# Kernel optimization log

Hardware: AMD Instinct MI355X
Metric: run time of the kernel (lower is better)

Reference implementation:

```python
import jax, jax.numpy as jnp
import numpy as np

HEAD_DIM = 64

def setup_inputs() -> dict:
    key = jax.random.key(0)
    k1, k2, k3 = jax.random.split(key, 3)
    B, L, D = 2, 2048, 1024
    x = jax.random.normal(k1, (B, L, D), dtype=jnp.float32)
    # torch nn.Linear weights are [out_features, in_features]
    w_qkv = jax.random.normal(k2, (3 * D, D), dtype=jnp.float32) * (D ** -0.5)
    w_out = jax.random.normal(k3, (D, D), dtype=jnp.float32) * (D ** -0.5)
    # causal mask: True = attend (masked_fill on logical_not)
    mask = jnp.tril(jnp.ones((L, L), dtype=bool))[None].repeat(B, axis=0)
    return {"x": x, "mask": mask, "w_qkv": w_qkv, "w_out": w_out}

def reference(x, mask, w_qkv, w_out):
    B, L, D = x.shape
    H, Hd = D // HEAD_DIM, HEAD_DIM
    scale = Hd ** -0.5
    qkv = x @ w_qkv.T                               # [B, L, 3D]
    q, k, v = jnp.split(qkv, 3, axis=-1)
    # [B, L, D] -> [B, H, L, Hd]
    def split_heads(t):
        return t.reshape(B, L, H, Hd).transpose(0, 2, 1, 3)
    q, k, v = split_heads(q), split_heads(k), split_heads(v)
    attn = jnp.einsum('bhld,bhmd->bhlm', q, k) * scale  # [B, H, L, L]
    attn = jnp.where(mask[:, None, :, :], attn, -jnp.inf)
    attn = jax.nn.softmax(attn, axis=-1)
    out = jnp.einsum('bhlm,bhmd->bhld', attn, v)        # [B, H, L, Hd]
    out = out.transpose(0, 2, 1, 3).reshape(B, L, D)
    return out @ w_out.T
```

## Files before the change

### kernel.cpp

```cpp
#include <hip/hip_runtime.h>
#include <hip/hip_bf16.h>


typedef __bf16 bf16;
typedef __bf16 bf16x8 __attribute__((ext_vector_type(8)));
typedef __bf16 bf16x4 __attribute__((ext_vector_type(4)));
typedef float  f32x4  __attribute__((ext_vector_type(4)));

#define MFMA16(a, b, c) __builtin_amdgcn_mfma_f32_16x16x32_bf16(a, b, c, 0, 0, 0)

__global__ __launch_bounds__(256) void cvt_all(
    const float* __restrict__ x, const float* __restrict__ wq,
    const float* __restrict__ wo, bf16* __restrict__ dst) {
  int i = blockIdx.x * 256 + threadIdx.x;
  const float* src;
  int off;
  if (i < 1048576) {
    src = x; off = i;
  } else if (i < 1048576 + 786432) {
    src = wq; off = i - 1048576;
  } else {
    src = wo; off = i - (1048576 + 786432);
  }
  float4 v = ((const float4*)src)[off];
  bf16x4 o;
  o[0] = (bf16)v.x; o[1] = (bf16)v.y; o[2] = (bf16)v.z; o[3] = (bf16)v.w;
  ((bf16x4*)dst)[i] = o;
}

__device__ __forceinline__ void gload_lds16(const bf16* g, bf16* l) {
  __builtin_amdgcn_global_load_lds(
      (const __attribute__((address_space(1))) void*)g,
      (__attribute__((address_space(3))) void*)l, 16, 0, 0);
}

template <int ROWS>
__device__ __forceinline__ void stage_tile(const bf16* __restrict__ src, int ld,
                                           bf16* lds, int tid) {
  const int wid = tid >> 6;
#pragma unroll
  for (int i = 0; i < ROWS / 32; ++i) {
    int c = i * 256 + tid;
    int row = c >> 3;
    int slot = (c & 7) ^ (row & 7);
    gload_lds16(src + row * ld + slot * 8, lds + i * 2048 + wid * 512);
  }
}

__device__ __forceinline__ void stage_tile512(const bf16* __restrict__ src,
                                              int ld, bf16* lds, int tid) {
  int row = tid >> 3;
  int slot = (tid & 7) ^ (row & 7);
  gload_lds16(src + row * ld + slot * 8, lds + (tid >> 6) * 512);
}

__device__ __forceinline__ bf16x8 read_swz(const bf16* lds, int row, int kbyte) {
  int byte = row * 128 + (kbyte ^ ((row & 7) << 4));
  return *(const bf16x8*)((const char*)lds + byte);
}

template <int MODE>
__global__ __launch_bounds__(256) void gemm_nt(
    const bf16* __restrict__ A, const bf16* __restrict__ Bt,
    bf16* __restrict__ C0, bf16* __restrict__ C1, bf16* __restrict__ C2,
    float* __restrict__ Cf,
    int M, int N, int K, int nbm) {
  __shared__ bf16 ldsA[128 * 64];
  __shared__ bf16 ldsB[128 * 64];
  const int tid = threadIdx.x;
  const int lane = tid & 63, wid = tid >> 6;
  const int wr = wid >> 1, wc = wid & 1;
  const int bm = blockIdx.x % nbm, bn = blockIdx.x / nbm;
  const int l15 = lane & 15, g = lane >> 4;

  f32x4 acc[4][4] = {};
  const bf16* Ab = A + (size_t)bm * 128 * K;
  const bf16* Bb = Bt + (size_t)bn * 128 * K;

  for (int k0 = 0; k0 < K; k0 += 64) {
    __syncthreads();
    stage_tile<128>(Ab + k0, K, ldsA, tid);
    stage_tile<128>(Bb + k0, K, ldsB, tid);
    __syncthreads();
#pragma unroll
    for (int kc = 0; kc < 2; ++kc) {
      bf16x8 af[4], bfr[4];
#pragma unroll
      for (int mi = 0; mi < 4; ++mi)
        af[mi] = read_swz(ldsA, wr * 64 + mi * 16 + l15, kc * 64 + g * 16);
#pragma unroll
      for (int ni = 0; ni < 4; ++ni)
        bfr[ni] = read_swz(ldsB, wc * 64 + ni * 16 + l15, kc * 64 + g * 16);
#pragma unroll
      for (int mi = 0; mi < 4; ++mi)
#pragma unroll
        for (int ni = 0; ni < 4; ++ni)
          acc[mi][ni] = MFMA16(af[mi], bfr[ni], acc[mi][ni]);
    }
  }

  const int mbase = bm * 128 + wr * 64, nbase = bn * 128 + wc * 64;
#pragma unroll
  for (int mi = 0; mi < 4; ++mi) {
#pragma unroll
    for (int ni = 0; ni < 4; ++ni) {
#pragma unroll
      for (int r = 0; r < 4; ++r) {
        int m = mbase + mi * 16 + g * 4 + r;
        int n = nbase + ni * 16 + l15;
        if (MODE == 0) {
          Cf[(size_t)m * N + n] = acc[mi][ni][r];
        } else {
          bf16 v = (bf16)acc[mi][ni][r];
          int part = n >> 10;
          int hh = (n >> 6) & 15, hd = n & 63;
          int bb = m >> 11, ll = m & 2047;
          size_t bhb = (size_t)(bb * 16 + hh);
          if (part == 2) {
            C2[(bhb * 64 + hd) * 2048 + ll] = v;
          } else {
            bf16* dst = (part == 0) ? C0 : C1;
            dst[(bhb * 2048 + ll) * 64 + hd] = v;
          }
        }
      }
    }
  }
}

__global__ __launch_bounds__(512) void attn_fwd8(
    const bf16* __restrict__ Q, const bf16* __restrict__ Kb,
    const bf16* __restrict__ Vt, bf16* __restrict__ O2) {
  __shared__ bf16 ldsK[2][64 * 64];
  __shared__ bf16 ldsVt[2][64 * 64];
  __shared__ bf16 ldsP[8 * 1024];

  const int tid = threadIdx.x, lane = tid & 63, wid = tid >> 6;
  const int l15 = lane & 15, g = lane >> 4;
  const int wsub = wid & 3;
  const int half = wid >> 2;
  const int qpair = 15 - (blockIdx.x >> 5);
  const int bh = blockIdx.x & 31;
  const int b = bh >> 4, h = bh & 15;
  const bf16* Qh  = Q  + (size_t)bh * 2048 * 64;
  const bf16* Kh  = Kb + (size_t)bh * 2048 * 64;
  const bf16* VtH = Vt + (size_t)bh * 64 * 2048;
  const int qbase = qpair * 128;
  const int qrow = qbase + half * 64 + wsub * 16 + l15;
  const int myqt = 2 * qpair + half;
  const int nt = 2 * qpair + 2;

  int off_rd[4][2];
#pragma unroll
  for (int r4 = 0; r4 < 4; ++r4)
#pragma unroll
    for (int dk = 0; dk < 2; ++dk)
      off_rd[r4][dk] = (r4 * 16 + l15) * 128 +
                       ((dk * 64 + g * 16) ^ ((l15 & 7) << 4));
  int off_pw[4];
#pragma unroll
  for (int s4 = 0; s4 < 4; ++s4)
    off_pw[s4] = l15 * 128 + ((s4 * 32 + g * 8) ^ ((l15 & 7) << 4));
  char* Pw = (char*)&ldsP[wid * 1024];

  bf16x8 qf[2];
#pragma unroll
  for (int dk = 0; dk < 2; ++dk)
    qf[dk] = *(const bf16x8*)(Qh + (size_t)qrow * 64 + dk * 32 + g * 8);

  float m_run = -__builtin_inff();
  float l_lane = 0.f;
  f32x4 oacc[4] = {};

  auto step = [&](bool masked, const char* Kt, const char* Vtt) {
    f32x4 s[4] = {};
#pragma unroll
    for (int sub = 0; sub < 4; ++sub) {
#pragma unroll
      for (int dk = 0; dk < 2; ++dk) {
        bf16x8 kf = *(const bf16x8*)(Kt + off_rd[sub][dk]);
        s[sub] = MFMA16(kf, qf[dk], s[sub]);
      }
    }
    if (masked) {
#pragma unroll
      for (int sub = 0; sub < 4; ++sub)
#pragma unroll
        for (int r = 0; r < 4; ++r) {
          int kvl = sub * 16 + g * 4 + r;
          if (kvl > wsub * 16 + l15) s[sub][r] = -__builtin_inff();
        }
    }
    float a0 = fmaxf(fmaxf(s[0][0], s[0][1]), s[0][2]);
    float a1 = fmaxf(fmaxf(s[0][3], s[1][0]), s[1][1]);
    float a2 = fmaxf(fmaxf(s[1][2], s[1][3]), s[2][0]);
    float a3 = fmaxf(fmaxf(s[2][1], s[2][2]), s[2][3]);
    float a4 = fmaxf(fmaxf(s[3][0], s[3][1]), s[3][2]);
    float lmax = fmaxf(fmaxf(fmaxf(a0, a1), fmaxf(a2, a3)),
                       fmaxf(a4, s[3][3]));
    if (!__all(lmax <= m_run)) {
      float mt = fmaxf(lmax, __shfl_xor(lmax, 16));
      mt = fmaxf(mt, __shfl_xor(mt, 32));
      float mnew = fmaxf(m_run, mt);
      float alpha = __expf(0.125f * (m_run - mnew));
#pragma unroll
      for (int dsub = 0; dsub < 4; ++dsub) {
        oacc[dsub][0] *= alpha; oacc[dsub][1] *= alpha;
        oacc[dsub][2] *= alpha; oacc[dsub][3] *= alpha;
      }
      l_lane *= alpha;
      m_run = mnew;
    }
    const float nms = -0.125f * m_run;
    float ls[4];
#pragma unroll
    for (int sub = 0; sub < 4; ++sub) {
      bf16x4 pb;
      float e0 = __expf(__builtin_fmaf(s[sub][0], 0.125f, nms));
      float e1 = __expf(__builtin_fmaf(s[sub][1], 0.125f, nms));
      float e2 = __expf(__builtin_fmaf(s[sub][2], 0.125f, nms));
      float e3 = __expf(__builtin_fmaf(s[sub][3], 0.125f, nms));
      pb[0] = (bf16)e0; pb[1] = (bf16)e1; pb[2] = (bf16)e2; pb[3] = (bf16)e3;
      ls[sub] = (e0 + e1) + (e2 + e3);
      *(bf16x4*)(Pw + off_pw[sub]) = pb;
    }
    l_lane += (ls[0] + ls[1]) + (ls[2] + ls[3]);
#pragma unroll
    for (int kc = 0; kc < 2; ++kc) {
      bf16x8 pf = *(const bf16x8*)(Pw + off_rd[0][kc]);
#pragma unroll
      for (int dsub = 0; dsub < 4; ++dsub) {
        bf16x8 vf = *(const bf16x8*)(Vtt + off_rd[dsub][kc]);
        oacc[dsub] = MFMA16(vf, pf, oacc[dsub]);
      }
    }
  };

  stage_tile512(Kh, 64, &ldsK[0][0], tid);
  stage_tile512(VtH, 2048, &ldsVt[0][0], tid);
  __syncthreads();

  int cur = 0;
  for (int t = 0; t < nt; ++t) {
    if (t + 1 < nt) {
      stage_tile512(Kh + (size_t)(t + 1) * 64 * 64, 64, &ldsK[cur ^ 1][0], tid);
      stage_tile512(VtH + (t + 1) * 64, 2048, &ldsVt[cur ^ 1][0], tid);
    }
    if (t <= myqt)
      step(t == myqt, (const char*)&ldsK[cur][0], (const char*)&ldsVt[cur][0]);
    __syncthreads();
    cur ^= 1;
  }

  float l_run = l_lane;
  l_run += __shfl_xor(l_run, 16);
  l_run += __shfl_xor(l_run, 32);
  const float linv = 1.f / l_run;
#pragma unroll
  for (int dsub = 0; dsub < 4; ++dsub)
#pragma unroll
    for (int r = 0; r < 4; ++r) {
      int d = dsub * 16 + g * 4 + r;
      O2[((size_t)(b * 2048 + qrow)) * 1024 + h * 64 + d] =
          (bf16)(oacc[dsub][r] * linv);
    }
}

extern "C" void kernel_launch(void* const* d_in, const int* in_sizes, int n_in,
                              void* d_out, int out_size, void* d_ws, size_t ws_size,
                              hipStream_t stream) {
  const float* x     = (const float*)d_in[0];
  const float* w_qkv = (const float*)d_in[2];
  const float* w_out = (const float*)d_in[3];
  float* out = (float*)d_out;

  char* ws = (char*)d_ws;
  bf16* xb    = (bf16*)(ws);
  bf16* wqkvb = (bf16*)(ws + ((size_t)8 << 20));
  bf16* woutb = (bf16*)(ws + ((size_t)14 << 20));
  bf16* Qb    = (bf16*)(ws + ((size_t)16 << 20));
  bf16* Kbuf  = (bf16*)(ws + ((size_t)24 << 20));
  bf16* Vtb   = (bf16*)(ws + ((size_t)32 << 20));
  bf16* O2    = (bf16*)(ws + ((size_t)40 << 20));

  cvt_all<<<dim3(8192), 256, 0, stream>>>(x, w_qkv, w_out, xb);

  gemm_nt<1><<<dim3(32 * 24), 256, 0, stream>>>(xb, wqkvb, Qb, Kbuf, Vtb,
                                                nullptr, 4096, 3072, 1024, 32);
  attn_fwd8<<<dim3(32 * 16), 512, 0, stream>>>(Qb, Kbuf, Vtb, O2);
  gemm_nt<0><<<dim3(32 * 8), 256, 0, stream>>>(O2, woutb, nullptr, nullptr,
                                               nullptr, out, 4096, 1024, 1024, 32);
}
```

Baseline: 203.2 us.

## Stage 128-row KV tiles per barrier and shrink per-wave P buffer

The attention kernel now stages 128-key K and V^T tiles per iteration instead of 64. This halves the number of loop iterations and block-wide barriers, and each wave runs two 64-key sub-steps per tile, ordered by wave parity to spread LDS bank pressure. The softmax P scratch is cut to a 16x32 slice written and consumed per kc chunk, and s_setprio hints are placed around the MFMA blocks. The block-to-qpair mapping changes so that blocks 256 and above handle queries in reverse order. This doubles K/V LDS use, which may lower occupancy, and the causal last-tile handling becomes more intricate.

```diff
diff --git a/kernel.cpp b/kernel.cpp
--- a/kernel.cpp
+++ b/kernel.cpp
@@ -47,11 +47,16 @@
   }
 }
 
-__device__ __forceinline__ void stage_tile512(const bf16* __restrict__ src,
-                                              int ld, bf16* lds, int tid) {
-  int row = tid >> 3;
-  int slot = (tid & 7) ^ (row & 7);
-  gload_lds16(src + row * ld + slot * 8, lds + (tid >> 6) * 512);
+template <int LOG2C>
+__device__ __forceinline__ void stage2_512(const bf16* __restrict__ src, int ld,
+                                           bf16* lds, int tid) {
+#pragma unroll
+  for (int i = 0; i < 2; ++i) {
+    int c = i * 512 + tid;
+    int row = c >> LOG2C;
+    int slot = (c & ((1 << LOG2C) - 1)) ^ (row & 7);
+    gload_lds16(src + row * ld + slot * 8, lds + i * 4096 + (tid >> 6) * 512);
+  }
 }
 
 __device__ __forceinline__ bf16x8 read_swz(const bf16* lds, int row, int kbyte) {
@@ -131,37 +136,42 @@
 __global__ __launch_bounds__(512) void attn_fwd8(
     const bf16* __restrict__ Q, const bf16* __restrict__ Kb,
     const bf16* __restrict__ Vt, bf16* __restrict__ O2) {
-  __shared__ bf16 ldsK[2][64 * 64];
-  __shared__ bf16 ldsVt[2][64 * 64];
-  __shared__ bf16 ldsP[8 * 1024];
+  __shared__ bf16 ldsK[2][128 * 64];
+  __shared__ bf16 ldsVt[2][64 * 128];
+  __shared__ bf16 ldsP[8][16 * 32];
 
   const int tid = threadIdx.x, lane = tid & 63, wid = tid >> 6;
   const int l15 = lane & 15, g = lane >> 4;
   const int wsub = wid & 3;
-  const int half = wid >> 2;
-  const int qpair = 15 - (blockIdx.x >> 5);
-  const int bh = blockIdx.x & 31;
+  const int hlf = wid >> 2;
+  const int bid = blockIdx.x;
+  const int qpair = (bid < 256) ? (15 - (bid >> 5)) : ((bid >> 5) - 8);
+  const int bh = bid & 31;
   const int b = bh >> 4, h = bh & 15;
   const bf16* Qh  = Q  + (size_t)bh * 2048 * 64;
   const bf16* Kh  = Kb + (size_t)bh * 2048 * 64;
   const bf16* VtH = Vt + (size_t)bh * 64 * 2048;
   const int qbase = qpair * 128;
-  const int qrow = qbase + half * 64 + wsub * 16 + l15;
-  const int myqt = 2 * qpair + half;
-  const int nt = 2 * qpair + 2;
-
-  int off_rd[4][2];
-#pragma unroll
-  for (int r4 = 0; r4 < 4; ++r4)
+  const int qrow = qbase + hlf * 64 + wsub * 16 + l15;
+  const int nt = qpair + 1;
+
+  int offK[4][2];
+#pragma unroll
+  for (int s4 = 0; s4 < 4; ++s4)
 #pragma unroll
     for (int dk = 0; dk < 2; ++dk)
-      off_rd[r4][dk] = (r4 * 16 + l15) * 128 +
-                       ((dk * 64 + g * 16) ^ ((l15 & 7) << 4));
-  int off_pw[4];
-#pragma unroll
-  for (int s4 = 0; s4 < 4; ++s4)
-    off_pw[s4] = l15 * 128 + ((s4 * 32 + g * 8) ^ ((l15 & 7) << 4));
-  char* Pw = (char*)&ldsP[wid * 1024];
+      offK[s4][dk] = (s4 * 16 + l15) * 128 +
+                     ((dk * 64 + g * 16) ^ ((l15 & 7) << 4));
+  int offV[4][2];
+#pragma unroll
+  for (int d4 = 0; d4 < 4; ++d4)
+#pragma unroll
+    for (int kc = 0; kc < 2; ++kc)
+      offV[d4][kc] = (d4 * 16 + l15) * 256 +
+                     ((kc * 64 + g * 16) ^ ((l15 & 7) << 4));
+  const int offPw0 = l15 * 64 + g * 8;
+  const int offPr  = l15 * 64 + g * 16;
+  char* Pw = (char*)&ldsP[wid][0];
 
   bf16x8 qf[2];
 #pragma unroll
@@ -172,32 +182,36 @@
   float l_lane = 0.f;
   f32x4 oacc[4] = {};
 
-  auto step = [&](bool masked, const char* Kt, const char* Vtt) {
-    f32x4 s[4] = {};
+  auto sub_step = [&](int s, bool masked, const char* Kt, const char* Vtt) {
+    const char* Ks = Kt + s * 8192;
+    const char* Vs = Vtt + s * 128;
+    f32x4 sv[4] = {};
+    __builtin_amdgcn_s_setprio(1);
 #pragma unroll
     for (int sub = 0; sub < 4; ++sub) {
 #pragma unroll
       for (int dk = 0; dk < 2; ++dk) {
-        bf16x8 kf = *(const bf16x8*)(Kt + off_rd[sub][dk]);
-        s[sub] = MFMA16(kf, qf[dk], s[sub]);
-      }
-    }
+        bf16x8 kf = *(const bf16x8*)(Ks + offK[sub][dk]);
+        sv[sub] = MFMA16(kf, qf[dk], sv[sub]);
+      }
+    }
+    __builtin_amdgcn_s_setprio(0);
     if (masked) {
 #pragma unroll
       for (int sub = 0; sub < 4; ++sub)
 #pragma unroll
         for (int r = 0; r < 4; ++r) {
           int kvl = sub * 16 + g * 4 + r;
-          if (kvl > wsub * 16 + l15) s[sub][r] = -__builtin_inff();
+          if (kvl > wsub * 16 + l15) sv[sub][r] = -__builtin_inff();
         }
     }
-    float a0 = fmaxf(fmaxf(s[0][0], s[0][1]), s[0][2]);
-    float a1 = fmaxf(fmaxf(s[0][3], s[1][0]), s[1][1]);
-    float a2 = fmaxf(fmaxf(s[1][2], s[1][3]), s[2][0]);
-    float a3 = fmaxf(fmaxf(s[2][1], s[2][2]), s[2][3]);
-    float a4 = fmaxf(fmaxf(s[3][0], s[3][1]), s[3][2]);
+    float a0 = fmaxf(fmaxf(sv[0][0], sv[0][1]), sv[0][2]);
+    float a1 = fmaxf(fmaxf(sv[0][3], sv[1][0]), sv[1][1]);
+    float a2 = fmaxf(fmaxf(sv[1][2], sv[1][3]), sv[2][0]);
+    float a3 = fmaxf(fmaxf(sv[2][1], sv[2][2]), sv[2][3]);
+    float a4 = fmaxf(fmaxf(sv[3][0], sv[3][1]), sv[3][2]);
     float lmax = fmaxf(fmaxf(fmaxf(a0, a1), fmaxf(a2, a3)),
-                       fmaxf(a4, s[3][3]));
+                       fmaxf(a4, sv[3][3]));
     if (!__all(lmax <= m_run)) {
       float mt = fmaxf(lmax, __shfl_xor(lmax, 16));
       mt = fmaxf(mt, __shfl_xor(mt, 32));
@@ -212,42 +226,55 @@
       m_run = mnew;
     }
     const float nms = -0.125f * m_run;
-    float ls[4];
-#pragma unroll
-    for (int sub = 0; sub < 4; ++sub) {
-      bf16x4 pb;
-      float e0 = __expf(__builtin_fmaf(s[sub][0], 0.125f, nms));
-      float e1 = __expf(__builtin_fmaf(s[sub][1], 0.125f, nms));
-      float e2 = __expf(__builtin_fmaf(s[sub][2], 0.125f, nms));
-      float e3 = __expf(__builtin_fmaf(s[sub][3], 0.125f, nms));
-      pb[0] = (bf16)e0; pb[1] = (bf16)e1; pb[2] = (bf16)e2; pb[3] = (bf16)e3;
-      ls[sub] = (e0 + e1) + (e2 + e3);
-      *(bf16x4*)(Pw + off_pw[sub]) = pb;
-    }
-    l_lane += (ls[0] + ls[1]) + (ls[2] + ls[3]);
 #pragma unroll
     for (int kc = 0; kc < 2; ++kc) {
-      bf16x8 pf = *(const bf16x8*)(Pw + off_rd[0][kc]);
+      float lsq = 0.f;
+#pragma unroll
+      for (int j = 0; j < 2; ++j) {
+        const f32x4& sj = sv[kc * 2 + j];
+        float e0 = __expf(__builtin_fmaf(sj[0], 0.125f, nms));
+        float e1 = __expf(__builtin_fmaf(sj[1], 0.125f, nms));
+        float e2 = __expf(__builtin_fmaf(sj[2], 0.125f, nms));
+        float e3 = __expf(__builtin_fmaf(sj[3], 0.125f, nms));
+        bf16x4 pb;
+        pb[0] = (bf16)e0; pb[1] = (bf16)e1; pb[2] = (bf16)e2; pb[3] = (bf16)e3;
+        lsq += (e0 + e1) + (e2 + e3);
+        *(bf16x4*)(Pw + offPw0 + j * 32) = pb;
+      }
+      l_lane += lsq;
+      bf16x8 pf = *(const bf16x8*)(Pw + offPr);
+      __builtin_amdgcn_s_setprio(1);
 #pragma unroll
       for (int dsub = 0; dsub < 4; ++dsub) {
-        bf16x8 vf = *(const bf16x8*)(Vtt + off_rd[dsub][kc]);
+        bf16x8 vf = *(const bf16x8*)(Vs + offV[dsub][kc]);
         oacc[dsub] = MFMA16(vf, pf, oacc[dsub]);
       }
+      __builtin_amdgcn_s_setprio(0);
     }
   };
 
-  stage_tile512(Kh, 64, &ldsK[0][0], tid);
-  stage_tile512(VtH, 2048, &ldsVt[0][0], tid);
+  stage2_512<3>(Kh, 64, &ldsK[0][0], tid);
+  stage2_512<4>(VtH, 2048, &ldsVt[0][0], tid);
   __syncthreads();
 
+  const int sf = wid & 1;
   int cur = 0;
   for (int t = 0; t < nt; ++t) {
     if (t + 1 < nt) {
-      stage_tile512(Kh + (size_t)(t + 1) * 64 * 64, 64, &ldsK[cur ^ 1][0], tid);
-      stage_tile512(VtH + (t + 1) * 64, 2048, &ldsVt[cur ^ 1][0], tid);
-    }
-    if (t <= myqt)
-      step(t == myqt, (const char*)&ldsK[cur][0], (const char*)&ldsVt[cur][0]);
+      stage2_512<3>(Kh + (size_t)(t + 1) * 128 * 64, 64, &ldsK[cur ^ 1][0], tid);
+      stage2_512<4>(VtH + (t + 1) * 128, 2048, &ldsVt[cur ^ 1][0], tid);
+    }
+    const char* Kt  = (const char*)&ldsK[cur][0];
+    const char* Vtt = (const char*)&ldsVt[cur][0];
+    if (t < nt - 1) {
+      sub_step(sf, false, Kt, Vtt);
+      sub_step(sf ^ 1, false, Kt, Vtt);
+    } else if (hlf == 0) {
+      sub_step(0, true, Kt, Vtt);
+    } else {
+      sub_step(sf, sf == 1, Kt, Vtt);
+      sub_step(sf ^ 1, (sf ^ 1) == 1, Kt, Vtt);
+    }
     __syncthreads();
     cur ^= 1;
   }
```

After: 202.7 us. Within noise of the previous version (-0.2%).
